# Kernel tuning notes

Hardware: AMD Instinct MI355X
Metric: run time of the kernel (lower is better)

The kernel has to match this reference:

```python
import jax, jax.numpy as jnp
import numpy as np

B, D, C = 1024, 512, 512


def _per_sample_ce(xi, yi, W, b):
    # categorical cross-entropy of a single sample through a linear+softmax head
    logits = xi @ W + b                      # [C]
    return -jnp.sum(yi * jax.nn.log_softmax(logits))


def setup_inputs() -> dict:
    key = jax.random.key(0)
    k1, k2, k3 = jax.random.split(key, 3)
    x = jax.random.normal(k1, (B, D), dtype=jnp.float32)
    labels = jax.random.randint(k2, (B,), 0, C)
    y_true = jax.nn.one_hot(labels, C, dtype=jnp.float32)  # [B, C]
    W = jax.random.normal(k3, (D, C), dtype=jnp.float32) * 0.02
    b = jnp.zeros((C,), dtype=jnp.float32)
    return {"x": x, "y_true": y_true, "W": W, "b": b}


def reference(x, y_true, W, b):
    # Per-sample gradient norm of the loss w.r.t. parameter_list = [W, b].
    # Equivalent to the Keras slow path (map_fn over samples of K.gradients),
    # vectorized with vmap over the batch dimension.
    def gnorm(xi, yi):
        gW, gb = jax.grad(lambda p: _per_sample_ce(xi, yi, p[0], p[1]))((W, b))
        return jnp.sqrt(jnp.sum(gW * gW) + jnp.sum(gb * gb))

    grads = jax.vmap(gnorm)(x, y_true)       # [B]
    return grads[:, None]                    # [B, 1] as in compute_output_shape
```

## Files before the change

### kernel.cpp

```cpp
#include <hip/hip_runtime.h>

#define Bn 1024
#define Dn 512
#define Cn 512

typedef __attribute__((ext_vector_type(8))) short s16x8;
typedef __attribute__((ext_vector_type(4))) float f32x4;
typedef __attribute__((ext_vector_type(4))) unsigned short u16x4;
typedef __attribute__((ext_vector_type(8))) unsigned short u16x8;

__device__ __forceinline__ unsigned short f2bf(float f) {
    unsigned u = __builtin_bit_cast(unsigned, f);
    u += 0x7FFF + ((u >> 16) & 1);
    return (unsigned short)(u >> 16);
}

__device__ __forceinline__ float waveSum(float v) {
    #pragma unroll
    for (int off = 32; off > 0; off >>= 1) v += __shfl_xor(v, off, 64);
    return v;
}

__global__ __launch_bounds__(256) void conv_kernel(const float* __restrict__ x,
                                                   const float* __restrict__ W,
                                                   unsigned short* __restrict__ xb,
                                                   unsigned short* __restrict__ wt)
{
    const int tid = threadIdx.x;
    if (blockIdx.x < 256) {
        const int base = (blockIdx.x * 256 + tid) * 8;
        float4 v0 = *(const float4*)&x[base];
        float4 v1 = *(const float4*)&x[base + 4];
        u16x8 o;
        o[0] = f2bf(v0.x); o[1] = f2bf(v0.y); o[2] = f2bf(v0.z); o[3] = f2bf(v0.w);
        o[4] = f2bf(v1.x); o[5] = f2bf(v1.y); o[6] = f2bf(v1.z); o[7] = f2bf(v1.w);
        *(u16x8*)&xb[base] = o;
    } else {
        __shared__ unsigned short lt[64][73];
        const int tb = blockIdx.x - 256;
        const int k0 = (tb >> 3) * 64, c0 = (tb & 7) * 64;
        const int rr = tid >> 4, cc = tid & 15;
        #pragma unroll
        for (int p = 0; p < 4; ++p) {
            const int kl = rr + p * 16;
            float4 v = *(const float4*)&W[(size_t)(k0 + kl) * Cn + c0 + cc * 4];
            lt[cc * 4 + 0][kl] = f2bf(v.x);
            lt[cc * 4 + 1][kl] = f2bf(v.y);
            lt[cc * 4 + 2][kl] = f2bf(v.z);
            lt[cc * 4 + 3][kl] = f2bf(v.w);
        }
        __syncthreads();
        #pragma unroll
        for (int p = 0; p < 4; ++p) {
            const int cl = rr + p * 16;
            u16x4 o;
            o[0] = lt[cl][cc * 4 + 0]; o[1] = lt[cl][cc * 4 + 1];
            o[2] = lt[cl][cc * 4 + 2]; o[3] = lt[cl][cc * 4 + 3];
            *(u16x4*)&wt[(size_t)(c0 + cl) * Dn + k0 + cc * 4] = o;
        }
    }
}

__global__ __launch_bounds__(512) void gnorm_mfma(
    const unsigned short* __restrict__ xb,
    const unsigned short* __restrict__ wt,
    const float* __restrict__ x,
    const float* __restrict__ y,
    const float* __restrict__ bias,
    float* __restrict__ out)
{
    __shared__ float lmax[16][8];
    __shared__ float lsum[16][8];
    __shared__ float lgsq[16][8];
    __shared__ float xn2s[16];

    const int tid = threadIdx.x;
    const int wv  = tid >> 6;
    const int l   = tid & 63;
    const int l15 = l & 15;
    const int lg  = l >> 4;
    const int s0  = blockIdx.x * 16;

    #pragma unroll
    for (int rr = 0; rr < 2; ++rr) {
        const int row = 2 * wv + rr;
        const float* xr = &x[(size_t)(s0 + row) * Dn + l * 8];
        float4 a = *(const float4*)xr;
        float4 b = *(const float4*)(xr + 4);
        float ss = a.x*a.x + a.y*a.y + a.z*a.z + a.w*a.w
                 + b.x*b.x + b.y*b.y + b.z*b.z + b.w*b.w;
        ss = waveSum(ss);
        if (l == 0) xn2s[row] = ss;
    }

    f32x4 acc[4];
    #pragma unroll
    for (int t = 0; t < 4; ++t) acc[t] = (f32x4){0.f, 0.f, 0.f, 0.f};

    const unsigned short* ap = &xb[(size_t)(s0 + l15) * Dn + lg * 8];
    const unsigned short* bp[4];
    #pragma unroll
    for (int t = 0; t < 4; ++t)
        bp[t] = &wt[(size_t)(wv * 64 + t * 16 + l15) * Dn + lg * 8];

    #pragma unroll
    for (int ks = 0; ks < 16; ++ks) {
        s16x8 a = *(const s16x8*)(ap + ks * 32);
        #pragma unroll
        for (int t = 0; t < 4; ++t) {
            s16x8 b = *(const s16x8*)(bp[t] + ks * 32);
            acc[t] = __builtin_amdgcn_mfma_f32_16x16x32_bf16(a, b, acc[t], 0, 0, 0);
        }
    }

    float bv[4];
    #pragma unroll
    for (int t = 0; t < 4; ++t) bv[t] = bias[wv * 64 + t * 16 + l15];

    float z[4][4];
    #pragma unroll
    for (int r = 0; r < 4; ++r)
        #pragma unroll
        for (int t = 0; t < 4; ++t) z[r][t] = acc[t][r] + bv[t];

    #pragma unroll
    for (int r = 0; r < 4; ++r) {
        float vm = fmaxf(fmaxf(z[r][0], z[r][1]), fmaxf(z[r][2], z[r][3]));
        #pragma unroll
        for (int off = 1; off < 16; off <<= 1) vm = fmaxf(vm, __shfl_xor(vm, off, 64));
        if (l15 == 0) lmax[lg * 4 + r][wv] = vm;
    }
    __syncthreads();

    float e[4][4];
    #pragma unroll
    for (int r = 0; r < 4; ++r) {
        const int m = lg * 4 + r;
        float vm = lmax[m][0];
        #pragma unroll
        for (int w = 1; w < 8; ++w) vm = fmaxf(vm, lmax[m][w]);
        float sv = 0.f;
        #pragma unroll
        for (int t = 0; t < 4; ++t) { e[r][t] = __expf(z[r][t] - vm); sv += e[r][t]; }
        #pragma unroll
        for (int off = 1; off < 16; off <<= 1) sv += __shfl_xor(sv, off, 64);
        if (l15 == 0) lsum[m][wv] = sv;
    }
    __syncthreads();

    #pragma unroll
    for (int r = 0; r < 4; ++r) {
        const int m = lg * 4 + r;
        float dv = 0.f;
        #pragma unroll
        for (int w = 0; w < 8; ++w) dv += lsum[m][w];
        const float inv = 1.0f / dv;
        float gs = 0.f;
        #pragma unroll
        for (int t = 0; t < 4; ++t) {
            float g = e[r][t] * inv - y[(size_t)(s0 + m) * Cn + wv * 64 + t * 16 + l15];
            gs += g * g;
        }
        #pragma unroll
        for (int off = 1; off < 16; off <<= 1) gs += __shfl_xor(gs, off, 64);
        if (l15 == 0) lgsq[m][wv] = gs;
    }
    __syncthreads();

    if (tid < 16) {
        float gsq = 0.f;
        #pragma unroll
        for (int w = 0; w < 8; ++w) gsq += lgsq[tid][w];
        out[s0 + tid] = sqrtf((xn2s[tid] + 1.0f) * gsq);
    }
}

extern "C" void kernel_launch(void* const* d_in, const int* in_sizes, int n_in,
                              void* d_out, int out_size, void* d_ws, size_t ws_size,
                              hipStream_t stream) {
    const float* x  = (const float*)d_in[0];
    const float* y  = (const float*)d_in[1];
    const float* W  = (const float*)d_in[2];
    const float* b  = (const float*)d_in[3];
    float* out = (float*)d_out;

    unsigned short* xb = (unsigned short*)d_ws;
    unsigned short* wt = (unsigned short*)((char*)d_ws + (size_t)Bn * Dn * 2);

    conv_kernel<<<dim3(256 + 64), dim3(256), 0, stream>>>(x, W, xb, wt);
    gnorm_mfma<<<dim3(Bn / 16), dim3(512), 0, stream>>>(xb, wt, x, y, b, out);
}
```

Before: 84.65 us.

## Fuse x bf16 conversion into GEMM kernel and stage W tiles through swizzled LDS

```diff
diff --git a/kernel.cpp b/kernel.cpp
--- a/kernel.cpp
+++ b/kernel.cpp
@@ -3,6 +3,8 @@
 #define Bn 1024
 #define Dn 512
 #define Cn 512
+#define KT 64
+#define NTL (Dn / KT)
 
 typedef __attribute__((ext_vector_type(8))) short s16x8;
 typedef __attribute__((ext_vector_type(4))) float f32x4;
@@ -15,64 +17,44 @@
     return (unsigned short)(u >> 16);
 }
 
-__device__ __forceinline__ float waveSum(float v) {
-    #pragma unroll
-    for (int off = 32; off > 0; off >>= 1) v += __shfl_xor(v, off, 64);
-    return v;
-}
-
-__global__ __launch_bounds__(256) void conv_kernel(const float* __restrict__ x,
-                                                   const float* __restrict__ W,
-                                                   unsigned short* __restrict__ xb,
-                                                   unsigned short* __restrict__ wt)
+__global__ __launch_bounds__(256) void wconv_kernel(const float* __restrict__ W,
+                                                    unsigned short* __restrict__ wt)
 {
+    __shared__ unsigned short lt[64][73];
     const int tid = threadIdx.x;
-    if (blockIdx.x < 256) {
-        const int base = (blockIdx.x * 256 + tid) * 8;
-        float4 v0 = *(const float4*)&x[base];
-        float4 v1 = *(const float4*)&x[base + 4];
-        u16x8 o;
-        o[0] = f2bf(v0.x); o[1] = f2bf(v0.y); o[2] = f2bf(v0.z); o[3] = f2bf(v0.w);
-        o[4] = f2bf(v1.x); o[5] = f2bf(v1.y); o[6] = f2bf(v1.z); o[7] = f2bf(v1.w);
-        *(u16x8*)&xb[base] = o;
-    } else {
-        __shared__ unsigned short lt[64][73];
-        const int tb = blockIdx.x - 256;
-        const int k0 = (tb >> 3) * 64, c0 = (tb & 7) * 64;
-        const int rr = tid >> 4, cc = tid & 15;
-        #pragma unroll
-        for (int p = 0; p < 4; ++p) {
-            const int kl = rr + p * 16;
-            float4 v = *(const float4*)&W[(size_t)(k0 + kl) * Cn + c0 + cc * 4];
-            lt[cc * 4 + 0][kl] = f2bf(v.x);
-            lt[cc * 4 + 1][kl] = f2bf(v.y);
-            lt[cc * 4 + 2][kl] = f2bf(v.z);
-            lt[cc * 4 + 3][kl] = f2bf(v.w);
-        }
-        __syncthreads();
-        #pragma unroll
-        for (int p = 0; p < 4; ++p) {
-            const int cl = rr + p * 16;
-            u16x4 o;
-            o[0] = lt[cl][cc * 4 + 0]; o[1] = lt[cl][cc * 4 + 1];
-            o[2] = lt[cl][cc * 4 + 2]; o[3] = lt[cl][cc * 4 + 3];
-            *(u16x4*)&wt[(size_t)(c0 + cl) * Dn + k0 + cc * 4] = o;
-        }
+    const int tb = blockIdx.x;
+    const int k0 = (tb >> 3) * 64, c0 = (tb & 7) * 64;
+    const int rr = tid >> 4, cc = tid & 15;
+    #pragma unroll
+    for (int p = 0; p < 4; ++p) {
+        const int kl = rr + p * 16;
+        float4 v = *(const float4*)&W[(size_t)(k0 + kl) * Cn + c0 + cc * 4];
+        lt[cc * 4 + 0][kl] = f2bf(v.x);
+        lt[cc * 4 + 1][kl] = f2bf(v.y);
+        lt[cc * 4 + 2][kl] = f2bf(v.z);
+        lt[cc * 4 + 3][kl] = f2bf(v.w);
+    }
+    __syncthreads();
+    #pragma unroll
+    for (int p = 0; p < 4; ++p) {
+        const int cl = rr + p * 16;
+        u16x4 o;
+        o[0] = lt[cl][cc * 4 + 0]; o[1] = lt[cl][cc * 4 + 1];
+        o[2] = lt[cl][cc * 4 + 2]; o[3] = lt[cl][cc * 4 + 3];
+        *(u16x4*)&wt[(size_t)(c0 + cl) * Dn + k0 + cc * 4] = o;
     }
 }
 
 __global__ __launch_bounds__(512) void gnorm_mfma(
-    const unsigned short* __restrict__ xb,
+    const float* __restrict__ x,
     const unsigned short* __restrict__ wt,
-    const float* __restrict__ x,
     const float* __restrict__ y,
     const float* __restrict__ bias,
     float* __restrict__ out)
 {
-    __shared__ float lmax[16][8];
-    __shared__ float lsum[16][8];
-    __shared__ float lgsq[16][8];
-    __shared__ float xn2s[16];
+    __shared__ unsigned short Ab[16 * 512];
+    __shared__ unsigned short Bb[2 * 512 * KT];
+    __shared__ float lmax[16 * 8], lsum[16 * 8], lgsq[16 * 8], xn2s[16];
 
     const int tid = threadIdx.x;
     const int wv  = tid >> 6;
@@ -81,42 +63,70 @@
     const int lg  = l >> 4;
     const int s0  = blockIdx.x * 16;
 
-    #pragma unroll
-    for (int rr = 0; rr < 2; ++rr) {
-        const int row = 2 * wv + rr;
-        const float* xr = &x[(size_t)(s0 + row) * Dn + l * 8];
-        float4 a = *(const float4*)xr;
-        float4 b = *(const float4*)(xr + 4);
-        float ss = a.x*a.x + a.y*a.y + a.z*a.z + a.w*a.w
-                 + b.x*b.x + b.y*b.y + b.z*b.z + b.w*b.w;
-        ss = waveSum(ss);
-        if (l == 0) xn2s[row] = ss;
-    }
+    {
+        const int row = tid >> 5, cs = tid & 31;
+        const float* xp = &x[(size_t)(s0 + row) * Dn + cs * 16];
+        float4 v0 = *(const float4*)xp,       v1 = *(const float4*)(xp + 4);
+        float4 v2 = *(const float4*)(xp + 8), v3 = *(const float4*)(xp + 12);
+        float ss = v0.x*v0.x + v0.y*v0.y + v0.z*v0.z + v0.w*v0.w
+                 + v1.x*v1.x + v1.y*v1.y + v1.z*v1.z + v1.w*v1.w
+                 + v2.x*v2.x + v2.y*v2.y + v2.z*v2.z + v2.w*v2.w
+                 + v3.x*v3.x + v3.y*v3.y + v3.z*v3.z + v3.w*v3.w;
+        u16x8 o0, o1;
+        o0[0]=f2bf(v0.x); o0[1]=f2bf(v0.y); o0[2]=f2bf(v0.z); o0[3]=f2bf(v0.w);
+        o0[4]=f2bf(v1.x); o0[5]=f2bf(v1.y); o0[6]=f2bf(v1.z); o0[7]=f2bf(v1.w);
+        o1[0]=f2bf(v2.x); o1[1]=f2bf(v2.y); o1[2]=f2bf(v2.z); o1[3]=f2bf(v2.w);
+        o1[4]=f2bf(v3.x); o1[5]=f2bf(v3.y); o1[6]=f2bf(v3.z); o1[7]=f2bf(v3.w);
+        char* base = (char*)Ab + row * 1024;
+        *(u16x8*)(base + (((2*cs    ) ^ (row & 7)) << 4)) = o0;
+        *(u16x8*)(base + (((2*cs + 1) ^ (row & 7)) << 4)) = o1;
+        #pragma unroll
+        for (int off = 1; off < 32; off <<= 1) ss += __shfl_xor(ss, off, 32);
+        if ((tid & 31) == 0) xn2s[row] = ss;
+    }
+
+    const int bc = (wv * 8) * 8 + (l >> 3);
+    const int kc = l & 7;
+    const int swz = (kc ^ (l >> 3)) << 4;
+#define STAGE_B(kt_, b_)                                                        \
+    {                                                                           \
+        _Pragma("unroll")                                                       \
+        for (int i = 0; i < 8; ++i) {                                           \
+            const int c = bc + i * 8;                                           \
+            u16x8 v = *(const u16x8*)&wt[(size_t)c * Dn + (kt_) * KT + kc * 8]; \
+            *(u16x8*)((char*)Bb + (b_) * (512 * KT * 2) + c * 128 + swz) = v;   \
+        }                                                                       \
+    }
+
+    STAGE_B(0, 0);
+    __syncthreads();
 
     f32x4 acc[4];
     #pragma unroll
     for (int t = 0; t < 4; ++t) acc[t] = (f32x4){0.f, 0.f, 0.f, 0.f};
 
-    const unsigned short* ap = &xb[(size_t)(s0 + l15) * Dn + lg * 8];
-    const unsigned short* bp[4];
-    #pragma unroll
-    for (int t = 0; t < 4; ++t)
-        bp[t] = &wt[(size_t)(wv * 64 + t * 16 + l15) * Dn + lg * 8];
-
-    #pragma unroll
-    for (int ks = 0; ks < 16; ++ks) {
-        s16x8 a = *(const s16x8*)(ap + ks * 32);
-        #pragma unroll
-        for (int t = 0; t < 4; ++t) {
-            s16x8 b = *(const s16x8*)(bp[t] + ks * 32);
-            acc[t] = __builtin_amdgcn_mfma_f32_16x16x32_bf16(a, b, acc[t], 0, 0, 0);
+    for (int kt = 0; kt < NTL; ++kt) {
+        if (kt + 1 < NTL) STAGE_B(kt + 1, (kt + 1) & 1);
+        const char* bbase = (const char*)Bb + (kt & 1) * (512 * KT * 2);
+        #pragma unroll
+        for (int ksl = 0; ksl < 2; ++ksl) {
+            const int ks = kt * 2 + ksl;
+            s16x8 a = *(const s16x8*)((char*)Ab + l15 * 1024 +
+                                      (((lg + ks * 4) ^ (l15 & 7)) << 4));
+            #pragma unroll
+            for (int t = 0; t < 4; ++t) {
+                const int c = wv * 64 + t * 16 + l15;
+                s16x8 bf = *(const s16x8*)(bbase + c * 128 +
+                                           (((lg + ksl * 4) ^ (l15 & 7)) << 4));
+                acc[t] = __builtin_amdgcn_mfma_f32_16x16x32_bf16(a, bf, acc[t], 0, 0, 0);
+            }
         }
+        __syncthreads();
     }
 
     float bv[4];
     #pragma unroll
     for (int t = 0; t < 4; ++t) bv[t] = bias[wv * 64 + t * 16 + l15];
-
     float z[4][4];
     #pragma unroll
     for (int r = 0; r < 4; ++r)
@@ -128,7 +138,7 @@
         float vm = fmaxf(fmaxf(z[r][0], z[r][1]), fmaxf(z[r][2], z[r][3]));
         #pragma unroll
         for (int off = 1; off < 16; off <<= 1) vm = fmaxf(vm, __shfl_xor(vm, off, 64));
-        if (l15 == 0) lmax[lg * 4 + r][wv] = vm;
+        if (l15 == 0) lmax[(lg * 4 + r) * 8 + wv] = vm;
     }
     __syncthreads();
 
@@ -136,15 +146,15 @@
     #pragma unroll
     for (int r = 0; r < 4; ++r) {
         const int m = lg * 4 + r;
-        float vm = lmax[m][0];
-        #pragma unroll
-        for (int w = 1; w < 8; ++w) vm = fmaxf(vm, lmax[m][w]);
+        float vm = lmax[m * 8];
+        #pragma unroll
+        for (int w = 1; w < 8; ++w) vm = fmaxf(vm, lmax[m * 8 + w]);
         float sv = 0.f;
         #pragma unroll
         for (int t = 0; t < 4; ++t) { e[r][t] = __expf(z[r][t] - vm); sv += e[r][t]; }
         #pragma unroll
         for (int off = 1; off < 16; off <<= 1) sv += __shfl_xor(sv, off, 64);
-        if (l15 == 0) lsum[m][wv] = sv;
+        if (l15 == 0) lsum[m * 8 + wv] = sv;
     }
     __syncthreads();
 
@@ -153,7 +163,7 @@
         const int m = lg * 4 + r;
         float dv = 0.f;
         #pragma unroll
-        for (int w = 0; w < 8; ++w) dv += lsum[m][w];
+        for (int w = 0; w < 8; ++w) dv += lsum[m * 8 + w];
         const float inv = 1.0f / dv;
         float gs = 0.f;
         #pragma unroll
@@ -163,14 +173,14 @@
         }
         #pragma unroll
         for (int off = 1; off < 16; off <<= 1) gs += __shfl_xor(gs, off, 64);
-        if (l15 == 0) lgsq[m][wv] = gs;
+        if (l15 == 0) lgsq[m * 8 + wv] = gs;
     }
     __syncthreads();
 
     if (tid < 16) {
         float gsq = 0.f;
         #pragma unroll
-        for (int w = 0; w < 8; ++w) gsq += lgsq[tid][w];
+        for (int w = 0; w < 8; ++w) gsq += lgsq[tid * 8 + w];
         out[s0 + tid] = sqrtf((xn2s[tid] + 1.0f) * gsq);
     }
 }
@@ -184,9 +194,8 @@
     const float* b  = (const float*)d_in[3];
     float* out = (float*)d_out;
 
-    unsigned short* xb = (unsigned short*)d_ws;
-    unsigned short* wt = (unsigned short*)((char*)d_ws + (size_t)Bn * Dn * 2);
-
-    conv_kernel<<<dim3(256 + 64), dim3(256), 0, stream>>>(x, W, xb, wt);
-    gnorm_mfma<<<dim3(Bn / 16), dim3(512), 0, stream>>>(xb, wt, x, y, b, out);
-}
+    unsigned short* wt = (unsigned short*)d_ws;
+
+    wconv_kernel<<<dim3(64), dim3(256), 0, stream>>>(W, wt);
+    gnorm_mfma<<<dim3(Bn / 16), dim3(512), 0, stream>>>(x, wt, y, b, out);
+}
```

Result: faster. 75.39 us (-10.9%).
